# Kernel tuning notes

Measured on AMD Instinct MI355X. Metric: run time of the kernel, lower is better.

Reference implementation:

```python
import jax, jax.numpy as jnp
import numpy as np

KS = 7          # kernel_size (odd)
STRIDE = 2
HALF = KS // 2  # window half-width
B, C, L = 32, 64, 4096


def setup_inputs() -> dict:
    key = jax.random.key(0)
    k1, k2 = jax.random.split(key)
    f = jax.random.normal(k1, (B, C, L), dtype=jnp.float32)
    # learned per-channel scale t ~ U(0, 4) (tiny epsilon to avoid div-by-zero)
    t = jax.random.uniform(k2, (C,), minval=0.0, maxval=4.0, dtype=jnp.float32) + 1e-3
    return {"f": f, "t": t}


def reference(f, t):
    b, c, n = f.shape
    # parabolic structuring function h[c, j] = -z_j^2 / (4 t_c), z = -HALF..HALF
    z = jnp.linspace(-HALF, HALF, KS, dtype=jnp.float32)
    h = -(z ** 2) / (4.0 * t[:, None])  # [C, KS]
    # morphological dilation (max-plus correlation) with -inf padding at borders
    pad = jnp.pad(f, ((0, 0), (0, 0), (HALF, HALF)), constant_values=-jnp.inf)
    out = pad[:, :, 0:n] + h[:, 0][None, :, None]
    for j in range(1, KS):  # small fixed KS-loop; fully vectorized over B,C,L
        out = jnp.maximum(out, pad[:, :, j:j + n] + h[:, j][None, :, None])
    # faithful reproduction of torch.as_strided(out, (B,C,L//stride), (1,1,stride))
    # on the contiguous buffer: element [b,c,i] = out_flat[b + c + i*stride]
    flat = out.reshape(-1)
    idx = (jnp.arange(b)[:, None, None]
           + jnp.arange(c)[None, :, None]
           + jnp.arange(n // STRIDE)[None, None, :] * STRIDE)
    return flat[idx]
```

## Files before the change

### kernel.cpp

```cpp
#include <hip/hip_runtime.h>
#include <math.h>


#define THREADS 256
#define NBLOCKS 2048
#define NFLAT   4189

__global__ __launch_bounds__(THREADS) void ParabolicPool1DFast_kernel(
    const float* __restrict__ f,
    const float* __restrict__ t,
    float* __restrict__ out)
{
    __shared__ __align__(16) float ev[2096];
    __shared__ __align__(16) float od[2096];

    const int tid = threadIdx.x;
    const float a0 = 0.25f / t[0];
    const float a1 = 0.25f / t[1];

    {
        const float4* f4 = (const float4*)f;
        float w[24];
        const int b0 = 4 * tid - 1;
#pragma unroll
        for (int v = 0; v < 6; ++v) {
            const int fi = b0 + v;
            const int fic = fi < 0 ? 0 : (fi > 1023 ? 1023 : fi);
            float4 x = f4[fic];
            if (fi < 0 || fi > 1023) {
                x.x = -INFINITY; x.y = -INFINITY; x.z = -INFINITY; x.w = -INFINITY;
            }
            w[4*v+0] = x.x; w[4*v+1] = x.y; w[4*v+2] = x.z; w[4*v+3] = x.w;
        }
        const float c1 = a0, c2 = 4.0f * a0, c3 = 9.0f * a0;
        float ve[8], vo[8];
#pragma unroll
        for (int p = 0; p < 16; ++p) {
            const float m1 = fmaxf(w[p+3], w[p+5]);
            const float m2 = fmaxf(w[p+2], w[p+6]);
            const float m3 = fmaxf(w[p+1], w[p+7]);
            const float val = fmaxf(fmaxf(w[p+4], m1 - c1),
                                    fmaxf(m2 - c2, m3 - c3));
            if (p & 1) vo[p >> 1] = val;
            else       ve[p >> 1] = val;
        }
        ((float4*)ev)[2*tid]     = make_float4(ve[0], ve[1], ve[2], ve[3]);
        ((float4*)ev)[2*tid + 1] = make_float4(ve[4], ve[5], ve[6], ve[7]);
        ((float4*)od)[2*tid]     = make_float4(vo[0], vo[1], vo[2], vo[3]);
        ((float4*)od)[2*tid + 1] = make_float4(vo[4], vo[5], vo[6], vo[7]);
    }

    if (tid < NFLAT - 4096) {
        const float* frow = f + 4096;
        float best = -INFINITY;
#pragma unroll
        for (int j = 0; j < 7; ++j) {
            const int z = j - 3;
            const int idx = tid + z;
            if (idx >= 0 && idx < 4096)
                best = fmaxf(best, frow[idx] - (float)(z * z) * a1);
        }
        const int q = 4096 + tid;
        if (q & 1) od[q >> 1] = best;
        else       ev[q >> 1] = best;
    }
    __syncthreads();

    const int r    = (int)blockIdx.x;
    const int base = (r >> 6) + (r & 63);
    const float* tab  = (base & 1) ? od : ev;
    const int    toff = base >> 1;
    float* orow = out + (r << 11);
#pragma unroll
    for (int k = 0; k < 2; ++k) {
        const int i = (k * THREADS + tid) * 4;
        const float4 v = make_float4(tab[toff + i],     tab[toff + i + 1],
                                     tab[toff + i + 2], tab[toff + i + 3]);
        *(float4*)(orow + i) = v;
    }
}

extern "C" void kernel_launch(void* const* d_in, const int* in_sizes, int n_in,
                              void* d_out, int out_size, void* d_ws, size_t ws_size,
                              hipStream_t stream) {
    const float* f = (const float*)d_in[0];
    const float* t = (const float*)d_in[1];
    float* out = (float*)d_out;
    ParabolicPool1DFast_kernel<<<NBLOCKS, THREADS, 0, stream>>>(f, t, out);
}
```

Before: 79.47 us.

## Compute dilation per output directly from global memory, removing shared table and barrier

Each block used to build the full dilated flat buffer (even and odd halves) in shared memory, synchronize, then gather its strided output row from it. Now each thread computes its four outputs directly from a 13-element global window, with a slow path for the row boundaries. This drops the per-block redundant table build, the shared-memory traffic and the __syncthreads. In exchange it issues many scalar, unaligned global loads per thread, which rely on L1/L2 hits because every block reads overlapping regions of the same small input.

```diff
diff --git a/kernel.cpp b/kernel.cpp
--- a/kernel.cpp
+++ b/kernel.cpp
@@ -4,79 +4,65 @@
 
 #define THREADS 256
 #define NBLOCKS 2048
-#define NFLAT   4189
 
 __global__ __launch_bounds__(THREADS) void ParabolicPool1DFast_kernel(
     const float* __restrict__ f,
     const float* __restrict__ t,
     float* __restrict__ out)
 {
-    __shared__ __align__(16) float ev[2096];
-    __shared__ __align__(16) float od[2096];
-
-    const int tid = threadIdx.x;
+    const int tid  = threadIdx.x;
+    const int r    = (int)blockIdx.x;
+    const int base = (r >> 6) + (r & 63);
     const float a0 = 0.25f / t[0];
     const float a1 = 0.25f / t[1];
+    const float c1 = a0, c2 = 4.0f * a0, c3 = 9.0f * a0;
+    float* orow = out + (r << 11);
 
-    {
-        const float4* f4 = (const float4*)f;
-        float w[24];
-        const int b0 = 4 * tid - 1;
-#pragma unroll
-        for (int v = 0; v < 6; ++v) {
-            const int fi = b0 + v;
-            const int fic = fi < 0 ? 0 : (fi > 1023 ? 1023 : fi);
-            float4 x = f4[fic];
-            if (fi < 0 || fi > 1023) {
-                x.x = -INFINITY; x.y = -INFINITY; x.z = -INFINITY; x.w = -INFINITY;
-            }
-            w[4*v+0] = x.x; w[4*v+1] = x.y; w[4*v+2] = x.z; w[4*v+3] = x.w;
-        }
-        const float c1 = a0, c2 = 4.0f * a0, c3 = 9.0f * a0;
-        float ve[8], vo[8];
-#pragma unroll
-        for (int p = 0; p < 16; ++p) {
-            const float m1 = fmaxf(w[p+3], w[p+5]);
-            const float m2 = fmaxf(w[p+2], w[p+6]);
-            const float m3 = fmaxf(w[p+1], w[p+7]);
-            const float val = fmaxf(fmaxf(w[p+4], m1 - c1),
-                                    fmaxf(m2 - c2, m3 - c3));
-            if (p & 1) vo[p >> 1] = val;
-            else       ve[p >> 1] = val;
-        }
-        ((float4*)ev)[2*tid]     = make_float4(ve[0], ve[1], ve[2], ve[3]);
-        ((float4*)ev)[2*tid + 1] = make_float4(ve[4], ve[5], ve[6], ve[7]);
-        ((float4*)od)[2*tid]     = make_float4(vo[0], vo[1], vo[2], vo[3]);
-        ((float4*)od)[2*tid + 1] = make_float4(vo[4], vo[5], vo[6], vo[7]);
-    }
-
-    if (tid < NFLAT - 4096) {
-        const float* frow = f + 4096;
-        float best = -INFINITY;
-#pragma unroll
-        for (int j = 0; j < 7; ++j) {
-            const int z = j - 3;
-            const int idx = tid + z;
-            if (idx >= 0 && idx < 4096)
-                best = fmaxf(best, frow[idx] - (float)(z * z) * a1);
-        }
-        const int q = 4096 + tid;
-        if (q & 1) od[q >> 1] = best;
-        else       ev[q >> 1] = best;
-    }
-    __syncthreads();
-
-    const int r    = (int)blockIdx.x;
-    const int base = (r >> 6) + (r & 63);
-    const float* tab  = (base & 1) ? od : ev;
-    const int    toff = base >> 1;
-    float* orow = out + (r << 11);
 #pragma unroll
     for (int k = 0; k < 2; ++k) {
-        const int i = (k * THREADS + tid) * 4;
-        const float4 v = make_float4(tab[toff + i],     tab[toff + i + 1],
-                                     tab[toff + i + 2], tab[toff + i + 3]);
-        *(float4*)(orow + i) = v;
+        const int i0 = (k * THREADS + tid) * 4;
+        const int q0 = base + 2 * i0;
+        const int p0 = q0 - 3;
+        float v0, v1, v2, v3;
+
+        if (p0 >= 0 && q0 + 9 <= 4095) {
+            float w[13];
+            const float* fp = f + p0;
+#pragma unroll
+            for (int v = 0; v < 13; ++v) w[v] = fp[v];
+            float r4[4];
+#pragma unroll
+            for (int j = 0; j < 4; ++j) {
+                const float m1 = fmaxf(w[2*j + 2], w[2*j + 4]);
+                const float m2 = fmaxf(w[2*j + 1], w[2*j + 5]);
+                const float m3 = fmaxf(w[2*j + 0], w[2*j + 6]);
+                r4[j] = fmaxf(fmaxf(w[2*j + 3], m1 - c1),
+                              fmaxf(m2 - c2, m3 - c3));
+            }
+            v0 = r4[0]; v1 = r4[1]; v2 = r4[2]; v3 = r4[3];
+        } else {
+            float r4[4];
+#pragma unroll
+            for (int j = 0; j < 4; ++j) {
+                const int q   = q0 + 2 * j;
+                const int row = q >> 12;
+                const int l   = q & 4095;
+                const float aq = row ? a1 : a0;
+                const float* frow = f + (row << 12);
+                float best = -INFINITY;
+#pragma unroll
+                for (int zj = 0; zj < 7; ++zj) {
+                    const int z  = zj - 3;
+                    const int li = l + z;
+                    if (li >= 0 && li < 4096)
+                        best = fmaxf(best, frow[li] - (float)(z * z) * aq);
+                }
+                r4[j] = best;
+            }
+            v0 = r4[0]; v1 = r4[1]; v2 = r4[2]; v3 = r4[3];
+        }
+
+        *(float4*)(orow + i0) = make_float4(v0, v1, v2, v3);
     }
 }
 
```

Result: slower. 81.37 us (+2.4%).
